# Kernel optimization log

Hardware: AMD Instinct MI355X
Metric: run time of the kernel (lower is better)

Reference implementation:

```python
import math
import jax, jax.numpy as jnp
import numpy as np

N_LAYER = 4
D = 256            # n_embd
NH = 4             # n_head
MLP_MULT = 128
VOCAB = 256
N = D * MLP_MULT // NH   # 8192 neurons per head
LN_EPS = 1e-5
TWO_PI = 2.0 * math.pi


def get_freqs(n, theta=2.0 ** 16):
    # quantize(arange(n), q=2) = floor(t/2)*2
    t = jnp.floor(jnp.arange(n, dtype=jnp.float32) / 2.0) * 2.0
    return 1.0 / theta ** (t / n) / TWO_PI


def layernorm(x):
    # nn.LayerNorm(D, elementwise_affine=False): plain normalization
    m = jnp.mean(x, axis=-1, keepdims=True)
    v = jnp.var(x, axis=-1, keepdims=True)
    return (x - m) / jnp.sqrt(v + LN_EPS)


def rope(phases, v):
    # v_rot interleaves (-v_odd, v_even) pairs
    v_rot = jnp.stack((-v[..., 1::2], v[..., ::2]), axis=-1).reshape(v.shape)
    p = (phases % 1.0) * TWO_PI
    return v * jnp.cos(p) + v_rot * jnp.sin(p)


def attention(x_sparse, x):
    # Q = K = x_sparse: (B, nh, T, N); V = x: (B, 1, T, D)
    T = x_sparse.shape[2]
    freqs = get_freqs(N).reshape(1, 1, 1, N)
    phases = jnp.arange(T, dtype=jnp.float32).reshape(1, 1, T, 1) * freqs
    QR = rope(phases, x_sparse)                       # (B, nh, T, N)
    scores = jnp.einsum('bhtn,bhsn->bhts', QR, QR)    # (B, nh, T, T)
    mask = jnp.tril(jnp.ones((T, T), dtype=bool), k=-1)  # strict lower tri
    scores = jnp.where(mask, scores, 0.0)
    return scores @ x                                 # (B, nh, T, D), V broadcast over heads


def bdh_forward(idx, embed, encoder, encoder_v, decoder, lm_head):
    B, T = idx.shape
    x = embed[idx][:, None]        # (B, 1, T, D)
    x = layernorm(x)
    dec = decoder.reshape(NH, N, D)
    for _ in range(N_LAYER):
        x_latent = jnp.einsum('btd,hdn->bhtn', x[:, 0], encoder)   # D -> N expand
        x_sparse = jax.nn.relu(x_latent)
        yKV = attention(x_sparse, x)                               # (B, nh, T, D)
        yKV = layernorm(yKV)
        y_latent = jnp.einsum('bhtd,hdn->bhtn', yKV, encoder_v)
        y_sparse = jax.nn.relu(y_latent)
        xy_sparse = x_sparse * y_sparse                            # gate
        yMLP = jnp.einsum('bhtn,hnd->btd', xy_sparse, dec)         # N -> D decode
        x = layernorm(x + yMLP[:, None])                           # residual + LN
    logits = x[:, 0] @ lm_head    # (B, T, vocab)
    return logits


def setup_inputs() -> dict:
    key = jax.random.key(0)
    k1, k2, k3, k4, k5, k6 = jax.random.split(key, 6)
    B, T = 2, 512
    std = 0.02
    return {
        'idx': jax.random.randint(k1, (B, T), 0, VOCAB, dtype=jnp.int64 if jax.config.jax_enable_x64 else jnp.int32),
        'embed': jax.random.normal(k2, (VOCAB, D), dtype=jnp.float32) * std,
        'encoder': jax.random.normal(k3, (NH, D, N), dtype=jnp.float32) * std,
        'encoder_v': jax.random.normal(k4, (NH, D, N), dtype=jnp.float32) * std,
        'decoder': jax.random.normal(k5, (NH * N, D), dtype=jnp.float32) * std,
        'lm_head': jax.random.normal(k6, (D, VOCAB), dtype=jnp.float32) * std,
    }


def reference(idx, embed, encoder, encoder_v, decoder, lm_head):
    return bdh_forward(idx, embed, encoder, encoder_v, decoder, lm_head)
```

## Files before the change

kernel.cpp:

```cpp
#include <hip/hip_runtime.h>
#include <hip/hip_bf16.h>
#include <cstdio>

#define DEV static __device__ __forceinline__

typedef __attribute__((ext_vector_type(4))) float floatx4;
typedef __attribute__((ext_vector_type(8))) __bf16 bf16x8;

constexpr int Bv = 2, Tv = 512, Dv = 256, NHv = 4, Nv = 8192, NLv = 4, Vv = 256;
constexpr int BTv = Bv * Tv;
constexpr int BHv = Bv * NHv;
constexpr float LNEPS = 1e-5f;
constexpr int KS_SC = 8;
constexpr int KS_DEC = 8;

DEV float b2f(short s) {
    unsigned u = ((unsigned)(unsigned short)s) << 16;
    return __builtin_bit_cast(float, u);
}
DEV short f2b(float f) {
    unsigned u = __builtin_bit_cast(unsigned, f);
    u = (u + 0x7fffu + ((u >> 16) & 1u)) >> 16;
    return (short)u;
}

__global__ __launch_bounds__(256) void k_cvtT(const float* __restrict__ in,
                                              short* __restrict__ out, int R, int C) {
    __shared__ float tile[32][33];
    const float* ib = in + (size_t)blockIdx.z * R * C;
    short* ob = out + (size_t)blockIdx.z * R * C;
    int c0 = blockIdx.x * 32, r0 = blockIdx.y * 32;
    int tx = threadIdx.x & 31, ty = threadIdx.x >> 5;
#pragma unroll
    for (int i = 0; i < 4; i++) {
        int r = r0 + ty + i * 8;
        tile[ty + i * 8][tx] = ib[(size_t)r * C + c0 + tx];
    }
    __syncthreads();
#pragma unroll
    for (int i = 0; i < 4; i++) {
        int c = c0 + ty + i * 8;
        ob[(size_t)c * R + r0 + tx] = f2b(tile[tx][ty + i * 8]);
    }
}

__global__ __launch_bounds__(256) void k_transp(const short* __restrict__ xb,
                                                short* __restrict__ xbT) {
    __shared__ short tile[32][33];
    int b = blockIdx.z;
    int t0 = blockIdx.x * 32, d0 = blockIdx.y * 32;
    int tx = threadIdx.x & 31, ty = threadIdx.x >> 5;
#pragma unroll
    for (int i = 0; i < 4; i++)
        tile[ty + i * 8][tx] = xb[((size_t)b * Tv + t0 + ty + i * 8) * Dv + d0 + tx];
    __syncthreads();
#pragma unroll
    for (int i = 0; i < 4; i++)
        xbT[((size_t)b * Dv + d0 + ty + i * 8) * Tv + t0 + tx] = tile[tx][ty + i * 8];
}

__global__ __launch_bounds__(256) void k_rope(unsigned* __restrict__ tab) {
    int i = blockIdx.x * 256 + threadIdx.x;
    int t = blockIdx.y;
    float f = exp2f(-(float)i / 256.0f) * 0.15915494309189535f;
    float ph = fmodf((float)t * f, 1.0f) * 6.2831853071795864f;
    unsigned c = (unsigned short)f2b(cosf(ph));
    unsigned s = (unsigned short)f2b(sinf(ph));
    tab[(size_t)t * (Nv / 2) + i] = c | (s << 16);
}

DEV void reduce2(float& s1, float& s2) {
    __shared__ float r1[4];
    __shared__ float r2[4];
#pragma unroll
    for (int o = 32; o > 0; o >>= 1) {
        s1 += __shfl_down(s1, o, 64);
        s2 += __shfl_down(s2, o, 64);
    }
    int lane = threadIdx.x & 63, w = threadIdx.x >> 6;
    if (lane == 0) { r1[w] = s1; r2[w] = s2; }
    __syncthreads();
    s1 = r1[0] + r1[1] + r1[2] + r1[3];
    s2 = r2[0] + r2[1] + r2[2] + r2[3];
}

DEV float ln_val(float v, float s1, float s2) {
    float m = s1 * (1.0f / Dv);
    float var = s2 * (1.0f / Dv) - m * m;
    float inv = rsqrtf(var + LNEPS);
    return (v - m) * inv;
}

__global__ __launch_bounds__(256) void k_embed_ln(const int* __restrict__ idx,
                                                  const float* __restrict__ embed,
                                                  float* __restrict__ xf, short* __restrict__ xb) {
    int r = blockIdx.x, d = threadIdx.x;
    float v = embed[(size_t)idx[r] * Dv + d];
    float s1 = v, s2 = v * v;
    reduce2(s1, s2);
    float o = ln_val(v, s1, s2);
    xf[(size_t)r * Dv + d] = o;
    xb[(size_t)r * Dv + d] = f2b(o);
}

__global__ __launch_bounds__(256) void k_ln(const float* __restrict__ in,
                                            short* __restrict__ outb) {
    int r = blockIdx.x, d = threadIdx.x;
    size_t o = (size_t)r * Dv + d;
    float v = in[o];
    float s1 = v, s2 = v * v;
    reduce2(s1, s2);
    outb[o] = f2b(ln_val(v, s1, s2));
}

__global__ __launch_bounds__(256) void k_lnsum(const short* __restrict__ ymb,
                                               float* __restrict__ xf, short* __restrict__ xb) {
    int r = blockIdx.x, d = threadIdx.x;
    size_t o = (size_t)r * Dv + d;
    float v = xf[o];
#pragma unroll
    for (int z = 0; z < NHv * KS_DEC; z++)
        v += b2f(ymb[(size_t)z * BTv * Dv + o]);
    float s1 = v, s2 = v * v;
    reduce2(s1, s2);
    float res = ln_val(v, s1, s2);
    xf[o] = res;
    xb[o] = f2b(res);
}

DEV void gemm_main(const short* __restrict__ Ab, int lda,
                   const short* __restrict__ Bb, int ldb, int K,
                   short* sA, short* sB, floatx4 acc[4][4]) {
    const int tid = threadIdx.x;
    const int lane = tid & 63, w = tid >> 6;
    const int wr = w >> 1, wc = w & 1;
    const int lrow = lane & 15, koff = (lane >> 4) * 8;
    for (int kk = 0; kk < K; kk += 32) {
        __syncthreads();
#pragma unroll
        for (int p = 0; p < 2; p++) {
            int c = tid + p * 256;
            int row = c >> 2, kc = c & 3;
            *(int4*)&sA[row * 40 + kc * 8] = *(const int4*)&Ab[(size_t)row * lda + kk + kc * 8];
            *(int4*)&sB[row * 40 + kc * 8] = *(const int4*)&Bb[(size_t)row * ldb + kk + kc * 8];
        }
        __syncthreads();
        bf16x8 aF[4], bF[4];
#pragma unroll
        for (int m = 0; m < 4; m++) aF[m] = *(const bf16x8*)&sA[(wr * 64 + m * 16 + lrow) * 40 + koff];
#pragma unroll
        for (int n = 0; n < 4; n++) bF[n] = *(const bf16x8*)&sB[(wc * 64 + n * 16 + lrow) * 40 + koff];
#pragma unroll
        for (int m = 0; m < 4; m++)
#pragma unroll
            for (int n = 0; n < 4; n++)
                acc[m][n] = __builtin_amdgcn_mfma_f32_16x16x32_bf16(aF[m], bF[n], acc[m][n], 0, 0, 0);
    }
}

__global__ __launch_bounds__(256) void k_latent(const short* __restrict__ xb,
                                                const short* __restrict__ encT,
                                                const unsigned* __restrict__ ropeT,
                                                short* __restrict__ qr) {
    __shared__ short sA[128 * 40];
    __shared__ short sB[128 * 40];
    int bid = blockIdx.x;
    int xcd = bid & 7, rr = bid >> 3;
    int cmb = xcd + 8 * (rr & 31);
    int mb = rr >> 5;
    int nb = cmb & 63, h = cmb >> 6;
    const short* Ab = xb + (size_t)mb * 128 * Dv;
    const short* Bb = encT + (size_t)h * Nv * Dv + (size_t)nb * 128 * Dv;
    floatx4 acc[4][4] = {};
    gemm_main(Ab, Dv, Bb, Dv, Dv, sA, sB, acc);
    int lane = threadIdx.x & 63, w = threadIdx.x >> 6, wr = w >> 1, wc = w & 1;
    int rb = (lane >> 4) * 4, cb = lane & 15;
    float sgn = (cb & 1) ? 1.0f : -1.0f;
#pragma unroll
    for (int m = 0; m < 4; m++)
#pragma unroll
        for (int n = 0; n < 4; n++) {
            int col = nb * 128 + wc * 64 + n * 16 + cb;
#pragma unroll
            for (int r = 0; r < 4; r++) {
                int row = mb * 128 + wr * 64 + m * 16 + rb + r;
                int b = row >> 9, t = row & 511;
                float v = acc[m][n][r];
                v = v > 0.f ? v : 0.f;
                float vp = __shfl_xor(v, 1);
                unsigned cs = ropeT[(size_t)t * (Nv / 2) + (col >> 1)];
                float c = b2f((short)(cs & 0xffff)), s = b2f((short)(cs >> 16));
                qr[((size_t)(b * NHv + h) * Tv + t) * Nv + col] = f2b(v * c + sgn * vp * s);
            }
        }
}

__global__ __launch_bounds__(256) void k_scores(const short* __restrict__ qr,
                                                short* __restrict__ scs) {
    __shared__ short sA[128 * 40];
    __shared__ short sB[128 * 40];
    int bid = blockIdx.x;
    int xcd = bid & 7, rr = bid >> 3;
    int cmb = xcd + 8 * (rr & 7);
    int pb = rr >> 3;
    int bh = cmb & 7, ks = cmb >> 3;
    int tb = 0;
    while (((tb + 1) * (tb + 2)) / 2 <= pb) tb++;
    int sb = pb - (tb * (tb + 1)) / 2;
    const bool diag = (tb == sb);
    const int KC = Nv / KS_SC;
    const short* Ab = qr + ((size_t)bh * Tv + tb * 128) * Nv + ks * KC;
    const short* Bb = qr + ((size_t)bh * Tv + sb * 128) * Nv + ks * KC;
    floatx4 acc[4][4] = {};
    const int tid = threadIdx.x, lane = tid & 63, w = tid >> 6;
    const int wr = w >> 1, wc = w & 1;
    const int lrow = lane & 15, koff = (lane >> 4) * 8;
    for (int kk = 0; kk < KC; kk += 32) {
        __syncthreads();
#pragma unroll
        for (int p = 0; p < 2; p++) {
            int c = tid + p * 256;
            int row = c >> 2, kc = c & 3;
            *(int4*)&sA[row * 40 + kc * 8] = *(const int4*)&Ab[(size_t)row * Nv + kk + kc * 8];
            if (!diag)
                *(int4*)&sB[row * 40 + kc * 8] = *(const int4*)&Bb[(size_t)row * Nv + kk + kc * 8];
        }
        __syncthreads();
        const short* sBr = diag ? sA : sB;
        bf16x8 aF[4], bF[4];
#pragma unroll
        for (int m = 0; m < 4; m++) aF[m] = *(const bf16x8*)&sA[(wr * 64 + m * 16 + lrow) * 40 + koff];
#pragma unroll
        for (int n = 0; n < 4; n++) bF[n] = *(const bf16x8*)&sBr[(wc * 64 + n * 16 + lrow) * 40 + koff];
#pragma unroll
        for (int m = 0; m < 4; m++)
#pragma unroll
            for (int n = 0; n < 4; n++)
                acc[m][n] = __builtin_amdgcn_mfma_f32_16x16x32_bf16(aF[m], bF[n], acc[m][n], 0, 0, 0);
    }
    short* slab = scs + ((size_t)ks * BHv + bh) * Tv * Tv;
    int rb = (lane >> 4) * 4, cb = lane & 15;
#pragma unroll
    for (int m = 0; m < 4; m++)
#pragma unroll
        for (int n = 0; n < 4; n++)
#pragma unroll
            for (int r = 0; r < 4; r++) {
                int t = tb * 128 + wr * 64 + m * 16 + rb + r;
                int s = sb * 128 + wc * 64 + n * 16 + cb;
                slab[(size_t)t * Tv + s] = f2b(acc[m][n][r]);
            }
}

__global__ __launch_bounds__(256) void k_redsc(const short* __restrict__ scs,
                                               short* __restrict__ scb) {
    int c = blockIdx.x * 256 + threadIdx.x;
    int row = c >> 6;
    int s0 = (c & 63) * 8;
    int t = row & (Tv - 1);
    float a[8] = {};
#pragma unroll
    for (int ks = 0; ks < KS_SC; ks++) {
        int4 raw = *(const int4*)&scs[((size_t)ks * BHv * Tv + row) * Tv + s0];
        const short* rs = (const short*)&raw;
#pragma unroll
        for (int j = 0; j < 8; j++) a[j] += b2f(rs[j]);
    }
    union { short s[8]; int4 v; } u;
#pragma unroll
    for (int j = 0; j < 8; j++) u.s[j] = (s0 + j < t) ? f2b(a[j]) : 0;
    *(int4*)&scb[(size_t)row * Tv + s0] = u.v;
}

__global__ __launch_bounds__(256) void k_pvg(const short* __restrict__ scb,
                                             const short* __restrict__ xbT,
                                             float* __restrict__ ykv) {
    __shared__ short sA[128 * 40];
    __shared__ short sB[128 * 40];
    int mb = blockIdx.x, nb = blockIdx.y, bh = blockIdx.z;
    int b = bh >> 2;
    const short* Ab = scb + ((size_t)bh * Tv + mb * 128) * Tv;
    const short* Bb = xbT + ((size_t)b * Dv + nb * 128) * Tv;
    floatx4 acc[4][4] = {};
    gemm_main(Ab, Tv, Bb, Tv, Tv, sA, sB, acc);
    int lane = threadIdx.x & 63, w = threadIdx.x >> 6, wr = w >> 1, wc = w & 1;
    int rb = (lane >> 4) * 4, cb = lane & 15;
#pragma unroll
    for (int m = 0; m < 4; m++)
#pragma unroll
        for (int n = 0; n < 4; n++)
#pragma unroll
            for (int r = 0; r < 4; r++) {
                int t = mb * 128 + wr * 64 + m * 16 + rb + r;
                int d = nb * 128 + wc * 64 + n * 16 + cb;
                ykv[((size_t)bh * Tv + t) * Dv + d] = acc[m][n][r];
            }
}

__global__ __launch_bounds__(256) void k_gate(const short* __restrict__ ykvb,
                                              const short* __restrict__ encvT,
                                              const short* __restrict__ qr,
                                              const unsigned* __restrict__ ropeT,
                                              short* __restrict__ xy) {
    __shared__ short sA[128 * 40];
    __shared__ short sB[128 * 40];
    int bid = blockIdx.x;
    int xcd = bid & 7, rr = bid >> 3;
    int cmb = xcd + 8 * (rr & 31);
    int wi = rr >> 5;
    int mb = wi & 3, bq = wi >> 2;
    int nb = cmb & 63, h = cmb >> 6;
    int bh = bq * NHv + h;
    const short* Ab = ykvb + ((size_t)bh * Tv + mb * 128) * Dv;
    const short* Bb = encvT + (size_t)h * Nv * Dv + (size_t)nb * 128 * Dv;
    floatx4 acc[4][4] = {};
    gemm_main(Ab, Dv, Bb, Dv, Dv, sA, sB, acc);
    int lane = threadIdx.x & 63, w = threadIdx.x >> 6, wr = w >> 1, wc = w & 1;
    int rb = (lane >> 4) * 4, cb = lane & 15;
    float sgn = (cb & 1) ? 1.0f : -1.0f;
#pragma unroll
    for (int m = 0; m < 4; m++)
#pragma unroll
        for (int n = 0; n < 4; n++) {
            int col = nb * 128 + wc * 64 + n * 16 + cb;
#pragma unroll
            for (int r = 0; r < 4; r++) {
                int t = mb * 128 + wr * 64 + m * 16 + rb + r;
                size_t idx = ((size_t)bh * Tv + t) * Nv + col;
                float qv = b2f(qr[idx]);
                float qp = b2f(qr[idx ^ 1]);
                unsigned cs = ropeT[(size_t)t * (Nv / 2) + (col >> 1)];
                float c = b2f((short)(cs & 0xffff)), s = b2f((short)(cs >> 16));
                float xsr = qv * c - sgn * qp * s;
                float v = acc[m][n][r];
                v = v > 0.f ? v : 0.f;
                xy[idx] = f2b(v * xsr);
            }
        }
}

__global__ __launch_bounds__(256) void k_decode(const short* __restrict__ xy,
                                                const short* __restrict__ decT,
                                                short* __restrict__ ymb) {
    __shared__ short sA[128 * 40];
    __shared__ short sB[128 * 40];
    int bid = blockIdx.x;
    int xcd = bid & 7, rr = bid >> 3;
    int cmb = xcd + 8 * (rr & 7);
    int mb = rr >> 3;
    int nb = cmb & 1, h = (cmb >> 1) & 3, ks = cmb >> 3;
    const int KC = Nv / KS_DEC;
    int row0 = mb * 128;
    int b = row0 >> 9, t0 = row0 & 511;
    const short* Ab = xy + ((size_t)(b * NHv + h) * Tv + t0) * Nv + ks * KC;
    const short* Bb = decT + (size_t)h * Dv * Nv + (size_t)nb * 128 * Nv + ks * KC;
    floatx4 acc[4][4] = {};
    gemm_main(Ab, Nv, Bb, Nv, KC, sA, sB, acc);
    short* slab = ymb + (size_t)(h * KS_DEC + ks) * BTv * Dv;
    int lane = threadIdx.x & 63, w = threadIdx.x >> 6, wr = w >> 1, wc = w & 1;
    int rb = (lane >> 4) * 4, cb = lane & 15;
#pragma unroll
    for (int m = 0; m < 4; m++)
#pragma unroll
        for (int n = 0; n < 4; n++)
#pragma unroll
            for (int r = 0; r < 4; r++) {
                int row = row0 + wr * 64 + m * 16 + rb + r;
                int col = nb * 128 + wc * 64 + n * 16 + cb;
                slab[(size_t)row * Dv + col] = f2b(acc[m][n][r]);
            }
}

__global__ __launch_bounds__(256) void k_head(const short* __restrict__ xb,
                                              const short* __restrict__ lmhT,
                                              float* __restrict__ out) {
    __shared__ short sA[128 * 40];
    __shared__ short sB[128 * 40];
    int mb = blockIdx.x, nb = blockIdx.y;
    const short* Ab = xb + (size_t)mb * 128 * Dv;
    const short* Bb = lmhT + (size_t)nb * 128 * Dv;
    floatx4 acc[4][4] = {};
    gemm_main(Ab, Dv, Bb, Dv, Dv, sA, sB, acc);
    int lane = threadIdx.x & 63, w = threadIdx.x >> 6, wr = w >> 1, wc = w & 1;
    int rb = (lane >> 4) * 4, cb = lane & 15;
#pragma unroll
    for (int m = 0; m < 4; m++)
#pragma unroll
        for (int n = 0; n < 4; n++)
#pragma unroll
            for (int r = 0; r < 4; r++) {
                int row = mb * 128 + wr * 64 + m * 16 + rb + r;
                int col = nb * 128 + wc * 64 + n * 16 + cb;
                out[(size_t)row * Vv + col] = acc[m][n][r];
            }
}

extern "C" void kernel_launch(void* const* d_in, const int* in_sizes, int n_in,
                              void* d_out, int out_size, void* d_ws, size_t ws_size,
                              hipStream_t stream) {
    const int* idx = (const int*)d_in[0];
    const float* embed = (const float*)d_in[1];
    const float* enc = (const float*)d_in[2];
    const float* encv = (const float*)d_in[3];
    const float* dec = (const float*)d_in[4];
    const float* lmh = (const float*)d_in[5];
    float* out = (float*)d_out;

    char* w = (char*)d_ws;
    size_t off = 0;
    auto alloc = [&](size_t bytes) -> void* {
        void* p = w + off;
        off = (off + bytes + 255) & ~(size_t)255;
        return p;
    };
    short* encT = (short*)alloc((size_t)NHv * Nv * Dv * 2);
    short* encvT = (short*)alloc((size_t)NHv * Nv * Dv * 2);
    short* decT = (short*)alloc((size_t)NHv * Dv * Nv * 2);
    short* lmhT = (short*)alloc((size_t)Vv * Dv * 2);
    unsigned* ropeT = (unsigned*)alloc((size_t)Tv * (Nv / 2) * 4);
    float* xf = (float*)alloc((size_t)BTv * Dv * 4);
    short* xb = (short*)alloc((size_t)BTv * Dv * 2);
    short* xbT = (short*)alloc((size_t)BTv * Dv * 2);
    short* xy = (short*)alloc((size_t)BHv * Tv * Nv * 2);
    short* qr = (short*)alloc((size_t)BHv * Tv * Nv * 2);
    short* scs = (short*)alloc((size_t)KS_SC * BHv * Tv * Tv * 2);
    short* scb = (short*)alloc((size_t)BHv * Tv * Tv * 2);
    float* ykvf = (float*)alloc((size_t)BHv * Tv * Dv * 4);
    short* ykvb = (short*)alloc((size_t)BHv * Tv * Dv * 2);
    short* ymb = (short*)alloc((size_t)NHv * KS_DEC * BTv * Dv * 2);
    if (off > ws_size) {
        fprintf(stderr, "BDH: workspace too small: need %zu, have %zu\n", off, ws_size);
        return;
    }

    k_cvtT<<<dim3(Nv / 32, Dv / 32, NHv), 256, 0, stream>>>(enc, encT, Dv, Nv);
    k_cvtT<<<dim3(Nv / 32, Dv / 32, NHv), 256, 0, stream>>>(encv, encvT, Dv, Nv);
    k_cvtT<<<dim3(Dv / 32, Nv / 32, NHv), 256, 0, stream>>>(dec, decT, Nv, Dv);
    k_cvtT<<<dim3(Vv / 32, Dv / 32, 1), 256, 0, stream>>>(lmh, lmhT, Dv, Vv);
    k_rope<<<dim3(Nv / 2 / 256, Tv), 256, 0, stream>>>(ropeT);
    k_embed_ln<<<BTv, 256, 0, stream>>>(idx, embed, xf, xb);

    for (int L = 0; L < NLv; L++) {
        k_latent<<<2048, 256, 0, stream>>>(xb, encT, ropeT, qr);
        k_transp<<<dim3(Tv / 32, Dv / 32, Bv), 256, 0, stream>>>(xb, xbT);
        k_scores<<<640, 256, 0, stream>>>(qr, scs);
        k_redsc<<<(BHv * Tv * Tv / 8) / 256, 256, 0, stream>>>(scs, scb);
        k_pvg<<<dim3(Tv / 128, Dv / 128, BHv), 256, 0, stream>>>(scb, xbT, ykvf);
        k_ln<<<BHv * Tv, 256, 0, stream>>>(ykvf, ykvb);
        k_gate<<<2048, 256, 0, stream>>>(ykvb, encvT, qr, ropeT, xy);
        k_decode<<<512, 256, 0, stream>>>(xy, decT, ymb);
        k_lnsum<<<BTv, 256, 0, stream>>>(ymb, xf, xb);
    }
    k_head<<<dim3(BTv / 128, Vv / 128), 256, 0, stream>>>(xb, lmhT, out);
}
```

Before: 854.1 us.

## Fuse score split-K reduction into PV GEMM, skip masked tiles, halve decode split-K

Removes the separate score-reduction kernel. The PV GEMM now sums the KS_SC bf16 partial score slabs and applies the causal mask while loading its A tile, and it stops the K loop at the diagonal block. The decode GEMM's split-K drops from 8 to 4 with a remapped grid, and the gate epilogue loads each q pair with a single 32-bit read. This cuts the scb write/read round trip and the launch, and skips upper-triangle work. The trade-off is a PV GEMM with no load pipelining and only 64 blocks, plus less parallelism in decode.

```diff
diff --git a/kernel.cpp b/kernel.cpp
--- a/kernel.cpp
+++ b/kernel.cpp
@@ -12,7 +12,7 @@
 constexpr int BHv = Bv * NHv;
 constexpr float LNEPS = 1e-5f;
 constexpr int KS_SC = 8;
-constexpr int KS_DEC = 8;
+constexpr int KS_DEC = 4;
 
 DEV float b2f(short s) {
     unsigned u = ((unsigned)(unsigned short)s) << 16;
@@ -252,38 +252,60 @@
             }
 }
 
-__global__ __launch_bounds__(256) void k_redsc(const short* __restrict__ scs,
-                                               short* __restrict__ scb) {
-    int c = blockIdx.x * 256 + threadIdx.x;
-    int row = c >> 6;
-    int s0 = (c & 63) * 8;
-    int t = row & (Tv - 1);
-    float a[8] = {};
-#pragma unroll
-    for (int ks = 0; ks < KS_SC; ks++) {
-        int4 raw = *(const int4*)&scs[((size_t)ks * BHv * Tv + row) * Tv + s0];
-        const short* rs = (const short*)&raw;
-#pragma unroll
-        for (int j = 0; j < 8; j++) a[j] += b2f(rs[j]);
-    }
-    union { short s[8]; int4 v; } u;
-#pragma unroll
-    for (int j = 0; j < 8; j++) u.s[j] = (s0 + j < t) ? f2b(a[j]) : 0;
-    *(int4*)&scb[(size_t)row * Tv + s0] = u.v;
-}
-
-__global__ __launch_bounds__(256) void k_pvg(const short* __restrict__ scb,
+__global__ __launch_bounds__(256) void k_pvg(const short* __restrict__ scs,
                                              const short* __restrict__ xbT,
                                              float* __restrict__ ykv) {
     __shared__ short sA[128 * 40];
     __shared__ short sB[128 * 40];
-    int mb = blockIdx.x, nb = blockIdx.y, bh = blockIdx.z;
+    int bid = blockIdx.x;
+    int xcd = bid & 7, rr = bid >> 3;
+    int nb = rr & 1, qhi = rr >> 1;
+    int q = xcd + 8 * qhi;
+    int mb = q & 3, bh = q >> 2;
     int b = bh >> 2;
-    const short* Ab = scb + ((size_t)bh * Tv + mb * 128) * Tv;
     const short* Bb = xbT + ((size_t)b * Dv + nb * 128) * Tv;
     floatx4 acc[4][4] = {};
-    gemm_main(Ab, Tv, Bb, Tv, Tv, sA, sB, acc);
-    int lane = threadIdx.x & 63, w = threadIdx.x >> 6, wr = w >> 1, wc = w & 1;
+    const int tid = threadIdx.x, lane = tid & 63, w = tid >> 6;
+    const int wr = w >> 1, wc = w & 1;
+    const int lrow = lane & 15, koff = (lane >> 4) * 8;
+    const int kmax = (mb + 1) * 128;
+    for (int kk = 0; kk < kmax; kk += 32) {
+        __syncthreads();
+#pragma unroll
+        for (int p = 0; p < 2; p++) {
+            int c = tid + p * 256;
+            int row = c >> 2, kc = c & 3;
+            {
+                int t = mb * 128 + row;
+                int s0 = kk + kc * 8;
+                size_t off = ((size_t)bh * Tv + t) * Tv + s0;
+                float a[8] = {};
+#pragma unroll
+                for (int ks = 0; ks < KS_SC; ks++) {
+                    int4 raw = *(const int4*)&scs[(size_t)ks * BHv * Tv * Tv + off];
+                    const short* rs = (const short*)&raw;
+#pragma unroll
+                    for (int j = 0; j < 8; j++) a[j] += b2f(rs[j]);
+                }
+                union { short s[8]; int4 v; } u;
+#pragma unroll
+                for (int j = 0; j < 8; j++) u.s[j] = (s0 + j < t) ? f2b(a[j]) : 0;
+                *(int4*)&sA[row * 40 + kc * 8] = u.v;
+            }
+            *(int4*)&sB[row * 40 + kc * 8] = *(const int4*)&Bb[(size_t)row * Tv + kk + kc * 8];
+        }
+        __syncthreads();
+        bf16x8 aF[4], bF[4];
+#pragma unroll
+        for (int m = 0; m < 4; m++) aF[m] = *(const bf16x8*)&sA[(wr * 64 + m * 16 + lrow) * 40 + koff];
+#pragma unroll
+        for (int n = 0; n < 4; n++) bF[n] = *(const bf16x8*)&sB[(wc * 64 + n * 16 + lrow) * 40 + koff];
+#pragma unroll
+        for (int m = 0; m < 4; m++)
+#pragma unroll
+            for (int n = 0; n < 4; n++)
+                acc[m][n] = __builtin_amdgcn_mfma_f32_16x16x32_bf16(aF[m], bF[n], acc[m][n], 0, 0, 0);
+    }
     int rb = (lane >> 4) * 4, cb = lane & 15;
 #pragma unroll
     for (int m = 0; m < 4; m++)
@@ -317,7 +339,8 @@
     gemm_main(Ab, Dv, Bb, Dv, Dv, sA, sB, acc);
     int lane = threadIdx.x & 63, w = threadIdx.x >> 6, wr = w >> 1, wc = w & 1;
     int rb = (lane >> 4) * 4, cb = lane & 15;
-    float sgn = (cb & 1) ? 1.0f : -1.0f;
+    int par = cb & 1;
+    float sgn = par ? 1.0f : -1.0f;
 #pragma unroll
     for (int m = 0; m < 4; m++)
 #pragma unroll
@@ -327,8 +350,10 @@
             for (int r = 0; r < 4; r++) {
                 int t = mb * 128 + wr * 64 + m * 16 + rb + r;
                 size_t idx = ((size_t)bh * Tv + t) * Nv + col;
-                float qv = b2f(qr[idx]);
-                float qp = b2f(qr[idx ^ 1]);
+                unsigned pq = *(const unsigned*)&qr[idx & ~(size_t)1];
+                float qlo = b2f((short)(pq & 0xffff)), qhi2 = b2f((short)(pq >> 16));
+                float qv = par ? qhi2 : qlo;
+                float qp = par ? qlo : qhi2;
                 unsigned cs = ropeT[(size_t)t * (Nv / 2) + (col >> 1)];
                 float c = b2f((short)(cs & 0xffff)), s = b2f((short)(cs >> 16));
                 float xsr = qv * c - sgn * qp * s;
@@ -346,9 +371,11 @@
     __shared__ short sB[128 * 40];
     int bid = blockIdx.x;
     int xcd = bid & 7, rr = bid >> 3;
-    int cmb = xcd + 8 * (rr & 7);
-    int mb = rr >> 3;
-    int nb = cmb & 1, h = (cmb >> 1) & 3, ks = cmb >> 3;
+    int nb = rr & 1;
+    int mb = (rr >> 1) & 7;
+    int hi = rr >> 4;
+    int hk = hi * 8 + xcd;
+    int h = hk & 3, ks = hk >> 2;
     const int KC = Nv / KS_DEC;
     int row0 = mb * 128;
     int b = row0 >> 9, t0 = row0 & 511;
@@ -424,7 +451,6 @@
     short* xy = (short*)alloc((size_t)BHv * Tv * Nv * 2);
     short* qr = (short*)alloc((size_t)BHv * Tv * Nv * 2);
     short* scs = (short*)alloc((size_t)KS_SC * BHv * Tv * Tv * 2);
-    short* scb = (short*)alloc((size_t)BHv * Tv * Tv * 2);
     float* ykvf = (float*)alloc((size_t)BHv * Tv * Dv * 4);
     short* ykvb = (short*)alloc((size_t)BHv * Tv * Dv * 2);
     short* ymb = (short*)alloc((size_t)NHv * KS_DEC * BTv * Dv * 2);
@@ -444,11 +470,10 @@
         k_latent<<<2048, 256, 0, stream>>>(xb, encT, ropeT, qr);
         k_transp<<<dim3(Tv / 32, Dv / 32, Bv), 256, 0, stream>>>(xb, xbT);
         k_scores<<<640, 256, 0, stream>>>(qr, scs);
-        k_redsc<<<(BHv * Tv * Tv / 8) / 256, 256, 0, stream>>>(scs, scb);
-        k_pvg<<<dim3(Tv / 128, Dv / 128, BHv), 256, 0, stream>>>(scb, xbT, ykvf);
+        k_pvg<<<64, 256, 0, stream>>>(scs, xbT, ykvf);
         k_ln<<<BHv * Tv, 256, 0, stream>>>(ykvf, ykvb);
         k_gate<<<2048, 256, 0, stream>>>(ykvb, encvT, qr, ropeT, xy);
-        k_decode<<<512, 256, 0, stream>>>(xy, decT, ymb);
+        k_decode<<<256, 256, 0, stream>>>(xy, decT, ymb);
         k_lnsum<<<BTv, 256, 0, stream>>>(ymb, xf, xb);
     }
     k_head<<<dim3(BTv / 128, Vv / 128), 256, 0, stream>>>(xb, lmhT, out);
```

Result: slower. 1.281 ms (+50.0%).
